# Optimization experiments

Hardware: AMD Instinct MI355X
Metric: run time of the kernel (lower is better)

The kernel has to match this reference:

```python
import jax, jax.numpy as jnp
import numpy as np

B, T, D, H = 4, 2048, 1024, 16
HD = D // H  # head_dim = 64

def setup_inputs() -> dict:
    key = jax.random.key(0)
    k1, k2, k3 = jax.random.split(key, 3)
    x = jax.random.normal(k1, (B, T, D), dtype=jnp.float32)
    Wqkv = jax.random.normal(k2, (D, 3 * D), dtype=jnp.float32) * (D ** -0.5)
    Wout = jax.random.normal(k3, (D, D), dtype=jnp.float32) * (D ** -0.5)
    return {"x": x, "Wqkv": Wqkv, "Wout": Wout}

def reference(x, Wqkv, Wout):
    Bb, Tt, C = x.shape
    qkv = x @ Wqkv  # [B,T,3D]
    qkv = qkv.reshape(Bb, Tt, 3, H, HD)
    q, k, v = qkv[:, :, 0], qkv[:, :, 1], qkv[:, :, 2]  # each [B,T,H,HD]
    scale = 1.0 / np.sqrt(HD)
    # scores [B,H,T,T]
    attn = jnp.einsum('bqhd,bkhd->bhqk', q, k) * scale
    causal = jnp.tril(jnp.ones((Tt, Tt), dtype=bool))
    attn = jnp.where(causal[None, None], attn, -jnp.inf)
    attn = jax.nn.softmax(attn, axis=-1)
    out = jnp.einsum('bhqk,bkhd->bqhd', attn, v).reshape(Bb, Tt, C)
    return out @ Wout
```

## Files before the change

### kernel.cpp

```cpp
#include <hip/hip_runtime.h>
#include <hip/hip_bf16.h>

#define T_SEQ 2048
#define NBATCH 4
#define NHEAD 16
#define HDIM 64
#define DMODEL 1024

typedef __bf16 bf16x8 __attribute__((ext_vector_type(8)));
typedef float f32x4 __attribute__((ext_vector_type(4)));
typedef float f32x16 __attribute__((ext_vector_type(16)));

__device__ __forceinline__ unsigned short f2bf(float f) {
  unsigned int u = __builtin_bit_cast(unsigned int, f);
  u += 0x7fffu + ((u >> 16) & 1u);
  return (unsigned short)(u >> 16);
}

__device__ __forceinline__ float fexp2(float x) {
  float r;
  asm("v_exp_f32 %0, %1" : "=v"(r) : "v"(x));
  return r;
}

__device__ __forceinline__ void async_cp16(void* lds, const void* g) {
  __builtin_amdgcn_global_load_lds((const __attribute__((address_space(1))) void*)g,
                                   (__attribute__((address_space(3))) void*)lds,
                                   16, 0, 0);
}

__global__ __launch_bounds__(256) void conv_bf16_k(const float* __restrict__ in,
                                                   unsigned short* __restrict__ out, int n) {
  int i = (blockIdx.x * 256 + threadIdx.x) * 4;
  if (i >= n) return;
  float4 v = *(const float4*)(in + i);
  ushort4 o;
  o.x = f2bf(v.x); o.y = f2bf(v.y); o.z = f2bf(v.z); o.w = f2bf(v.w);
  *(ushort4*)(out + i) = o;
}

__global__ __launch_bounds__(256) void transpose_bf16_k(const float* __restrict__ in,
                                                        unsigned short* __restrict__ out,
                                                        int R, int C) {
  __shared__ float tile[32][33];
  int c0 = blockIdx.x * 32, r0 = blockIdx.y * 32;
  int tx = threadIdx.x, ty = threadIdx.y;
#pragma unroll
  for (int j = 0; j < 32; j += 8)
    tile[ty + j][tx] = in[(size_t)(r0 + ty + j) * C + c0 + tx];
  __syncthreads();
#pragma unroll
  for (int j = 0; j < 32; j += 8)
    out[(size_t)(c0 + ty + j) * R + r0 + tx] = f2bf(tile[tx][ty + j]);
}

__global__ __launch_bounds__(512, 1) void gemm1_v3_k(const unsigned short* __restrict__ A,
                                                     const unsigned short* __restrict__ Bt,
                                                     unsigned short* __restrict__ Qb,
                                                     unsigned short* __restrict__ Kb,
                                                     unsigned short* __restrict__ Vt) {
  __shared__ uint4 ldsv[7168];
  char* lds = (char*)ldsv;
  const int t = threadIdx.x;
  const int w = t >> 6, lane = t & 63;
  const int lr = lane & 15, lg = lane >> 4;
  const int wr = w >> 1, wc = w & 1;
  const int bid = blockIdx.x;
  const int wid = (bid & 7) * 64 + (bid >> 3);
  const int m0 = (wid >> 4) * 256, n0 = (wid & 15) * 192;

  const int row0 = t >> 3;
  const int colc0 = (t & 7) ^ (row0 & 7);
  const int stU = w * 1024;

  const unsigned short* Abase = A + (size_t)(m0 + row0) * 1024 + colc0 * 8;
  const unsigned short* Bbase = Bt + (size_t)(n0 + row0) * 1024 + colc0 * 8;

#define STGA(pb, h, kt)                                                          \
  async_cp16(lds + (pb) + (h) * 8192 + stU,                                      \
             Abase + (size_t)(h) * 64 * 1024 + (kt) * 64)
#define STGB(pb, s, kt)                                                          \
  async_cp16(lds + (pb) + 32768 + (s) * 8192 + stU,                              \
             Bbase + (size_t)(s) * 64 * 1024 + (kt) * 64)
#define VM3() asm volatile("s_waitcnt vmcnt(3)" ::: "memory")
#define BAR()                                                                    \
  {                                                                              \
    __builtin_amdgcn_s_barrier();                                                \
    __builtin_amdgcn_sched_barrier(0);                                           \
  }

  f32x4 acc[4][6];
#pragma unroll
  for (int mi = 0; mi < 4; ++mi)
#pragma unroll
    for (int ni = 0; ni < 6; ++ni) acc[mi][ni] = (f32x4){0.f, 0.f, 0.f, 0.f};

  STGA(0, 0, 0); STGA(0, 1, 0); STGA(0, 2, 0); STGA(0, 3, 0);
  STGB(0, 0, 0); STGB(0, 1, 0); STGB(0, 2, 0);
  STGB(57344, 0, 1); STGB(57344, 1, 1); STGB(57344, 2, 1);
  VM3();
  BAR();

  bf16x8 bfr[6][2], af[2];

#define LDB(pb)                                                                      \
  {                                                                                  \
    _Pragma("unroll") for (int ni = 0; ni < 6; ++ni) _Pragma("unroll")               \
        for (int kk = 0; kk < 2; ++kk) {                                             \
      int rrow = wc * 96 + ni * 16 + lr;                                             \
      int cc = (kk * 4 + lg) ^ (lr & 7);                                             \
      bfr[ni][kk] = *(const bf16x8*)(lds + (pb) + 32768 + rrow * 128 + cc * 16);     \
    }                                                                                \
  }
#define LDA(Q, pb)                                                                   \
  {                                                                                  \
    _Pragma("unroll") for (int kk = 0; kk < 2; ++kk) {                               \
      int rrow = wr * 64 + (Q) * 16 + lr;                                            \
      int cc = (kk * 4 + lg) ^ (lr & 7);                                             \
      af[kk] = *(const bf16x8*)(lds + (pb) + rrow * 128 + cc * 16);                  \
    }                                                                                \
  }
#define MM(Q)                                                                        \
  {                                                                                  \
    __builtin_amdgcn_s_setprio(1);                                                   \
    _Pragma("unroll") for (int kk = 0; kk < 2; ++kk) _Pragma("unroll")               \
        for (int ni = 0; ni < 6; ++ni) acc[Q][ni] =                                  \
            __builtin_amdgcn_mfma_f32_16x16x32_bf16(af[kk], bfr[ni][kk],             \
                                                    acc[Q][ni], 0, 0, 0);            \
    __builtin_amdgcn_s_setprio(0);                                                   \
  }

  const int P0 = 0, P1 = 57344;
  for (int I = 0; I < 8; ++I) {
    const int t1 = 2 * I + 1;
    const int t2 = (2 * I + 2 < 16) ? 2 * I + 2 : 15;
    const int t3 = (2 * I + 3 < 16) ? 2 * I + 3 : 15;
    LDB(P0); LDA(0, P0); STGA(P1, 0, t1); STGA(P1, 1, t1); BAR(); MM(0); BAR();
    LDA(1, P0); STGA(P1, 2, t1); STGA(P1, 3, t1); BAR(); MM(1); BAR();
    LDA(2, P0); STGB(P0, 0, t2); STGB(P0, 1, t2); BAR(); MM(2); BAR();
    LDA(3, P0); STGB(P0, 2, t2); BAR(); MM(3);
    VM3();
    BAR();
    LDB(P1); LDA(0, P1); STGA(P0, 0, t2); STGA(P0, 1, t2); BAR(); MM(0); BAR();
    LDA(1, P1); STGA(P0, 2, t2); STGA(P0, 3, t2); BAR(); MM(1); BAR();
    LDA(2, P1); STGB(P1, 0, t3); STGB(P1, 1, t3); BAR(); MM(2); BAR();
    LDA(3, P1); STGB(P1, 2, t3); BAR(); MM(3);
    VM3();
    BAR();
  }

#pragma unroll
  for (int mi = 0; mi < 4; ++mi) {
#pragma unroll
    for (int ni = 0; ni < 6; ++ni) {
      int gm = m0 + wr * 64 + mi * 16 + lg * 4;
      int gn = n0 + wc * 96 + ni * 16 + lr;
      f32x4 v = acc[mi][ni];
      int b = gm >> 11, tt = gm & 2047;
      int sel = gn >> 10, rem = gn & 1023;
      int h = rem >> 6, hd = rem & 63;
      int bh = b * NHEAD + h;
      if (sel == 0) {
        unsigned short* p = Qb + ((size_t)bh * T_SEQ + tt) * HDIM + hd;
#pragma unroll
        for (int r = 0; r < 4; ++r)
          p[(size_t)r * HDIM] = f2bf(v[r] * (0.125f * 1.44269504f));
      } else if (sel == 1) {
        unsigned short* p = Kb + (size_t)bh * T_SEQ * HDIM + (tt >> 5) * 2048 +
                            (hd >> 4) * 512 + ((hd >> 3) & 1) * 256 + (tt & 31) * 8 +
                            (hd & 7);
#pragma unroll
        for (int r = 0; r < 4; ++r) p[r * 8] = f2bf(v[r]);
      } else {
        unsigned short* p = Vt + (size_t)bh * T_SEQ * HDIM + (tt >> 4) * 1024 +
                            ((tt >> 3) & 1) * 512 + (hd >> 5) * 256 + (hd & 31) * 8 +
                            (tt & 7);
        ushort4 o;
        o.x = f2bf(v[0]); o.y = f2bf(v[1]); o.z = f2bf(v[2]); o.w = f2bf(v[3]);
        *(ushort4*)p = o;
      }
    }
  }
#undef STGA
#undef STGB
#undef VM3
#undef BAR
#undef LDB
#undef LDA
#undef MM
}

template <int EPI, int NT>
__global__ __launch_bounds__(512, 1) void gemm_8ph2_k(const unsigned short* __restrict__ A,
                                                      const unsigned short* __restrict__ Bt,
                                                      unsigned short* __restrict__ Qb,
                                                      unsigned short* __restrict__ Kb,
                                                      unsigned short* __restrict__ Vt,
                                                      float* __restrict__ Cout) {
  __shared__ uint4 ldsv[6144];
  char* lds = (char*)ldsv;
  const int t = threadIdx.x;
  const int w = t >> 6, lane = t & 63;
  const int lr = lane & 15, lg = lane >> 4;
  const int wr = w >> 1, wc = w & 1;
  const int bid = blockIdx.x;
  const int perx = (NT * 32) / 8;
  const int wid = (bid & 7) * perx + (bid >> 3);
  const int m0 = (wid / NT) * 256, n0 = (wid % NT) * 128;

  const int row0 = t >> 3;
  const int colc0 = (t & 7) ^ (row0 & 7);
  const int stU = w * 1024;

  const unsigned short* Abase = A + (size_t)(m0 + row0) * 1024 + colc0 * 8;
  const unsigned short* Bbase = Bt + (size_t)(n0 + row0) * 1024 + colc0 * 8;

#define STGA(dst, h, kt)                                                        \
  {                                                                             \
    const unsigned short* _s = Abase + (size_t)(h) * 128 * 1024 + (kt) * 64;    \
    async_cp16(lds + (dst) + (h) * 16384 + stU, _s);                            \
    async_cp16(lds + (dst) + (h) * 16384 + stU + 8192, _s + 64 * 1024);         \
  }
#define STGB(dst, kt)                                                           \
  {                                                                             \
    const unsigned short* _s = Bbase + (kt) * 64;                               \
    async_cp16(lds + (dst) + 32768 + stU, _s);                                  \
    async_cp16(lds + (dst) + 32768 + stU + 8192, _s + 64 * 1024);               \
  }
#define VM2() asm volatile("s_waitcnt vmcnt(2)" ::: "memory")
#define BAR()                                                                   \
  {                                                                             \
    __builtin_amdgcn_s_barrier();                                               \
    __builtin_amdgcn_sched_barrier(0);                                          \
  }

  f32x4 acc[4][4];
#pragma unroll
  for (int mi = 0; mi < 4; ++mi)
#pragma unroll
    for (int ni = 0; ni < 4; ++ni) acc[mi][ni] = (f32x4){0.f, 0.f, 0.f, 0.f};

  STGA(0, 0, 0);
  STGA(0, 1, 0);
  STGB(0, 0);
  STGB(49152, 1);
  VM2();
  BAR();

  bf16x8 bfr[4][2], af[2][2];
  const int ldsAh = (wr >> 1) * 16384;
  const int arow0 = (wr & 1) * 64;
  const int brow0 = wc * 64;

#define LDB(pbase)                                                                   \
  {                                                                                  \
    _Pragma("unroll") for (int ni = 0; ni < 4; ++ni) _Pragma("unroll")               \
        for (int kk = 0; kk < 2; ++kk) {                                             \
      int rrow = brow0 + ni * 16 + lr;                                               \
      int cc = (kk * 4 + lg) ^ (lr & 7);                                             \
      bfr[ni][kk] = *(const bf16x8*)(lds + (pbase) + 32768 + rrow * 128 + cc * 16);  \
    }                                                                                \
  }
#define LDA(Q, pbase)                                                                \
  {                                                                                  \
    _Pragma("unroll") for (int m2 = 0; m2 < 2; ++m2) _Pragma("unroll")               \
        for (int kk = 0; kk < 2; ++kk) {                                             \
      int rrow = arow0 + (2 * (Q) + m2) * 16 + lr;                                   \
      int cc = (kk * 4 + lg) ^ (lr & 7);                                             \
      af[m2][kk] = *(const bf16x8*)(lds + (pbase) + ldsAh + rrow * 128 + cc * 16);   \
    }                                                                                \
  }
#define MM(Q)                                                                        \
  {                                                                                  \
    __builtin_amdgcn_s_setprio(1);                                                   \
    _Pragma("unroll") for (int m2 = 0; m2 < 2; ++m2) _Pragma("unroll")               \
        for (int kk = 0; kk < 2; ++kk) _Pragma("unroll") for (int ni = 0; ni < 4;    \
                                                              ++ni) acc[2 * (Q) +    \
                                                                        m2][ni] =    \
            __builtin_amdgcn_mfma_f32_16x16x32_bf16(af[m2][kk], bfr[ni][kk],         \
                                                    acc[2 * (Q) + m2][ni], 0, 0, 0); \
    __builtin_amdgcn_s_setprio(0);                                                   \
  }

  for (int I = 0; I < 8; ++I) {
    const int t1o = 2 * I + 1;
    const int t2e = (2 * I + 2 < 16) ? 2 * I + 2 : 15;
    const int t3o = (2 * I + 3 < 16) ? 2 * I + 3 : 15;
    LDB(0); LDA(0, 0); STGA(49152, 0, t1o); BAR(); MM(0); BAR();
    LDA(1, 0); STGA(49152, 1, t1o); STGB(0, t2e); BAR(); MM(1); VM2(); BAR();
    LDB(49152); LDA(0, 49152); STGA(0, 0, t2e); BAR(); MM(0); BAR();
    LDA(1, 49152); STGA(0, 1, t2e); STGB(49152, t3o); BAR(); MM(1); VM2(); BAR();
  }

#pragma unroll
  for (int mi = 0; mi < 4; ++mi) {
#pragma unroll
    for (int ni = 0; ni < 4; ++ni) {
      int gm = m0 + wr * 64 + mi * 16 + lg * 4;
      int gn = n0 + wc * 64 + ni * 16 + lr;
      f32x4 v = acc[mi][ni];
#pragma unroll
      for (int r = 0; r < 4; ++r) Cout[(size_t)(gm + r) * (NT * 128) + gn] = v[r];
    }
  }
#undef STGA
#undef STGB
#undef VM2
#undef BAR
#undef LDB
#undef LDA
#undef MM
}

#define PVJJ(Sv, B, JJ, Oa, Obb)                                                              \
  {                                                                                           \
    unsigned w0, w1, w2, w3;                                                                  \
    asm("v_cvt_pk_bf16_f32 %0, %1, %2" : "=v"(w0) : "v"(Sv[B + 0]), "v"(Sv[B + 1]));          \
    asm("v_cvt_pk_bf16_f32 %0, %1, %2" : "=v"(w1) : "v"(Sv[B + 2]), "v"(Sv[B + 3]));          \
    asm("v_cvt_pk_bf16_f32 %0, %1, %2" : "=v"(w2) : "v"(Sv[B + 4]), "v"(Sv[B + 5]));          \
    asm("v_cvt_pk_bf16_f32 %0, %1, %2" : "=v"(w3) : "v"(Sv[B + 6]), "v"(Sv[B + 7]));          \
    asm("v_permlane32_swap_b32 %0, %1" : "+v"(w0), "+v"(w2));                                 \
    asm("v_permlane32_swap_b32 %0, %1" : "+v"(w1), "+v"(w3));                                 \
    union { unsigned u[4]; bf16x8 v; } pf;                                                    \
    pf.u[0] = w0; pf.u[1] = w1; pf.u[2] = w2; pf.u[3] = w3;                                   \
    bf16x8 vfa = *(const bf16x8*)(bv + (JJ) * 2048 + hi * 1024 + lq * 16);                    \
    bf16x8 vfb = *(const bf16x8*)(bv + (JJ) * 2048 + hi * 1024 + lq * 16 + 512);              \
    __builtin_amdgcn_s_setprio(1);                                                            \
    Oa = __builtin_amdgcn_mfma_f32_32x32x16_bf16(vfa, pf.v, Oa, 0, 0, 0);                     \
    Obb = __builtin_amdgcn_mfma_f32_32x32x16_bf16(vfb, pf.v, Obb, 0, 0, 0);                   \
    __builtin_amdgcn_s_setprio(0);                                                            \
  }

__global__ __launch_bounds__(512, 2) void attn_fwd9_k(const unsigned short* __restrict__ Qb,
                                                      const unsigned short* __restrict__ Kb,
                                                      const unsigned short* __restrict__ Vt,
                                                      unsigned short* __restrict__ Ob) {
  __shared__ char lds[32768];
  const int tid = threadIdx.x;
  const int w = tid >> 6, lane = tid & 63;
  const int lq = lane & 31, hi = lane >> 5;
  const int bid = blockIdx.x;
  const int xcd = bid & 7, i = bid >> 3;
  const int bh = xcd * 8 + (i & 7);
  const int s = (i < 32) ? 7 - (i >> 3) : (i >> 3) - 4;
  const int qb = s * 8 + w;
  const int qw = qb * 32;
  const int P = 4 * (s + 1);

  const unsigned short* Qp = Qb + (size_t)bh * T_SEQ * HDIM;
  const char* Ksrc = (const char*)(Kb + (size_t)bh * T_SEQ * HDIM);
  const char* Vsrc = (const char*)(Vt + (size_t)bh * T_SEQ * HDIM);
  const int b = bh >> 4, h = bh & 15;

#define ASTG(bb, p)                                                                  \
  {                                                                                  \
    async_cp16(lds + (bb) * 16384 + w * 1024, Ksrc + (size_t)(p) * 8192 + tid * 16); \
    async_cp16(lds + (bb) * 16384 + 8192 + w * 1024,                                 \
               Vsrc + (size_t)(p) * 8192 + tid * 16);                                \
  }

  bf16x8 qf[4];
#pragma unroll
  for (int dj = 0; dj < 4; ++dj)
    qf[dj] = *(const bf16x8*)(Qp + (size_t)(qw + lq) * HDIM + dj * 16 + hi * 8);

  f32x16 O0, O1;
#pragma unroll
  for (int r = 0; r < 16; ++r) { O0[r] = 0.f; O1[r] = 0.f; }
  float m_run = -30000.0f, l_run = 0.f;

  auto smax_pair = [&](f32x16& S0, f32x16& S1) {
    float m8[8];
#pragma unroll
    for (int r = 0; r < 8; ++r)
      m8[r] = fmaxf(fmaxf(S0[r], S0[r + 8]), fmaxf(S1[r], S1[r + 8]));
#pragma unroll
    for (int r = 0; r < 4; ++r) m8[r] = fmaxf(m8[r], m8[r + 4]);
    float pmax = fmaxf(fmaxf(m8[0], m8[1]), fmaxf(m8[2], m8[3]));
    pmax = fmaxf(pmax, __shfl_xor(pmax, 32, 64));
    if (__any(pmax > m_run + 11.5f)) {
      float mn = fmaxf(m_run, pmax);
      float al = fexp2(m_run - mn);
      m_run = mn;
      l_run *= al;
#pragma unroll
      for (int r = 0; r < 16; ++r) { O0[r] *= al; O1[r] *= al; }
    }
#pragma unroll
    for (int r = 0; r < 16; ++r) {
      S0[r] = fexp2(S0[r] - m_run);
      S1[r] = fexp2(S1[r] - m_run);
    }
    float s8[8];
#pragma unroll
    for (int r = 0; r < 8; ++r) s8[r] = (S0[r] + S0[r + 8]) + (S1[r] + S1[r + 8]);
#pragma unroll
    for (int r = 0; r < 4; ++r) s8[r] += s8[r + 4];
    float ps = (s8[0] + s8[1]) + (s8[2] + s8[3]);
    ps += __shfl_xor(ps, 32, 64);
    l_run += ps;
  };

  auto smax_single = [&](f32x16& S0) {
    float m8[8];
#pragma unroll
    for (int r = 0; r < 8; ++r) m8[r] = fmaxf(S0[r], S0[r + 8]);
#pragma unroll
    for (int r = 0; r < 4; ++r) m8[r] = fmaxf(m8[r], m8[r + 4]);
    float pmax = fmaxf(fmaxf(m8[0], m8[1]), fmaxf(m8[2], m8[3]));
    pmax = fmaxf(pmax, __shfl_xor(pmax, 32, 64));
    if (__any(pmax > m_run + 11.5f)) {
      float mn = fmaxf(m_run, pmax);
      float al = fexp2(m_run - mn);
      m_run = mn;
      l_run *= al;
#pragma unroll
      for (int r = 0; r < 16; ++r) { O0[r] *= al; O1[r] *= al; }
    }
#pragma unroll
    for (int r = 0; r < 16; ++r) S0[r] = fexp2(S0[r] - m_run);
    float s8[8];
#pragma unroll
    for (int r = 0; r < 8; ++r) s8[r] = S0[r] + S0[r + 8];
#pragma unroll
    for (int r = 0; r < 4; ++r) s8[r] += s8[r + 4];
    float ps = (s8[0] + s8[1]) + (s8[2] + s8[3]);
    ps += __shfl_xor(ps, 32, 64);
    l_run += ps;
  };

  ASTG(0, 0);
  __syncthreads();

  for (int p = 0; p < P; ++p) {
    if (p + 1 < P) ASTG((p + 1) & 1, p + 1);
    const char* bk = lds + (p & 1) * 16384;
    const char* bv = bk + 8192;
    const int t0 = 2 * p, t1 = 2 * p + 1;
    if (t0 <= qb) {
      const bool v1 = (t1 <= qb);
      f32x16 S0, S1;
#pragma unroll
      for (int r = 0; r < 16; ++r) { S0[r] = 0.f; S1[r] = 0.f; }
      __builtin_amdgcn_s_setprio(1);
#pragma unroll
      for (int dj = 0; dj < 4; ++dj) {
        bf16x8 k0 = *(const bf16x8*)(bk + dj * 1024 + lane * 16);
        S0 = __builtin_amdgcn_mfma_f32_32x32x16_bf16(k0, qf[dj], S0, 0, 0, 0);
      }
      if (v1) {
#pragma unroll
        for (int dj = 0; dj < 4; ++dj) {
          bf16x8 k1 = *(const bf16x8*)(bk + 4096 + dj * 1024 + lane * 16);
          S1 = __builtin_amdgcn_mfma_f32_32x32x16_bf16(k1, qf[dj], S1, 0, 0, 0);
        }
      }
      __builtin_amdgcn_s_setprio(0);
      if (t0 == qb) {
#pragma unroll
        for (int r = 0; r < 16; ++r) {
          int kvl = (r & 3) + 8 * (r >> 2) + 4 * hi;
          S0[r] = (kvl > lq) ? -30000.0f : S0[r];
        }
      }
      if (v1 && t1 == qb) {
#pragma unroll
        for (int r = 0; r < 16; ++r) {
          int kvl = (r & 3) + 8 * (r >> 2) + 4 * hi;
          S1[r] = (kvl > lq) ? -30000.0f : S1[r];
        }
      }
      if (v1) {
        smax_pair(S0, S1);
        PVJJ(S0, 0, 0, O0, O1); PVJJ(S0, 8, 1, O0, O1);
        PVJJ(S1, 0, 2, O0, O1); PVJJ(S1, 8, 3, O0, O1);
      } else {
        smax_single(S0);
        PVJJ(S0, 0, 0, O0, O1); PVJJ(S0, 8, 1, O0, O1);
      }
    }
    __syncthreads();
  }

  const float linv = 1.0f / l_run;
  unsigned short* op = Ob + ((size_t)(b * T_SEQ + qw + lq)) * DMODEL + h * HDIM;
#pragma unroll
  for (int g = 0; g < 4; ++g) {
    ushort4 o;
    o.x = f2bf(O0[4 * g + 0] * linv);
    o.y = f2bf(O0[4 * g + 1] * linv);
    o.z = f2bf(O0[4 * g + 2] * linv);
    o.w = f2bf(O0[4 * g + 3] * linv);
    *(ushort4*)(op + 8 * g + 4 * hi) = o;
    ushort4 o2;
    o2.x = f2bf(O1[4 * g + 0] * linv);
    o2.y = f2bf(O1[4 * g + 1] * linv);
    o2.z = f2bf(O1[4 * g + 2] * linv);
    o2.w = f2bf(O1[4 * g + 3] * linv);
    *(ushort4*)(op + 32 + 8 * g + 4 * hi) = o2;
  }
#undef ASTG
}

extern "C" void kernel_launch(void* const* d_in, const int* in_sizes, int n_in,
                              void* d_out, int out_size, void* d_ws, size_t ws_size,
                              hipStream_t stream) {
  const float* x = (const float*)d_in[0];
  const float* Wqkv = (const float*)d_in[1];
  const float* Wout = (const float*)d_in[2];
  float* out = (float*)d_out;

  unsigned short* ws = (unsigned short*)d_ws;
  const size_t nx = (size_t)NBATCH * T_SEQ * DMODEL;
  unsigned short* xb    = ws;
  unsigned short* wqkvT = xb + nx;
  unsigned short* woutT = wqkvT + (size_t)3 * DMODEL * DMODEL;
  unsigned short* Qb    = woutT + (size_t)DMODEL * DMODEL;
  unsigned short* Kb    = Qb + nx;
  unsigned short* Vt    = Kb + nx;
  unsigned short* Ab    = Vt + nx;
  size_t need = 2ull * (5 * nx + 4ull * DMODEL * DMODEL);
  if (ws_size < need) return;

  conv_bf16_k<<<dim3((unsigned)(nx / 1024)), dim3(256), 0, stream>>>(x, xb, (int)nx);
  transpose_bf16_k<<<dim3(3 * DMODEL / 32, DMODEL / 32), dim3(32, 8), 0, stream>>>(
      Wqkv, wqkvT, DMODEL, 3 * DMODEL);
  transpose_bf16_k<<<dim3(DMODEL / 32, DMODEL / 32), dim3(32, 8), 0, stream>>>(
      Wout, woutT, DMODEL, DMODEL);
  gemm1_v3_k<<<dim3(512), dim3(512), 0, stream>>>(xb, wqkvT, Qb, Kb, Vt);
  attn_fwd9_k<<<dim3(512), dim3(512), 0, stream>>>(Qb, Kb, Vt, Ab);
  gemm_8ph2_k<1, 8><<<dim3(256), dim3(512), 0, stream>>>(Ab, woutT, nullptr, nullptr,
                                                         nullptr, out);
}
```

Measured before the change: 146.5 us.

## Merge prep kernels into one launch and halve barrier phases in QKV GEMM

The three preprocessing launches (x conversion to bf16 and the two weight transpose-conversions) are folded into a single kernel whose block index selects the job, removing two launch gaps. The QKV projection GEMM main loop is restructured from four barrier-separated MFMA phases per buffer to two, double-buffering A fragments so two M-subtiles are loaded and multiplied per phase. This cuts barrier count and groups the global-to-LDS stage issues, at the cost of extra registers for the second A fragment set and less fine-grained interleaving of loads with compute.

```diff
diff --git a/kernel.cpp b/kernel.cpp
--- a/kernel.cpp
+++ b/kernel.cpp
@@ -29,22 +29,36 @@
                                    16, 0, 0);
 }
 
-__global__ __launch_bounds__(256) void conv_bf16_k(const float* __restrict__ in,
-                                                   unsigned short* __restrict__ out, int n) {
-  int i = (blockIdx.x * 256 + threadIdx.x) * 4;
-  if (i >= n) return;
-  float4 v = *(const float4*)(in + i);
-  ushort4 o;
-  o.x = f2bf(v.x); o.y = f2bf(v.y); o.z = f2bf(v.z); o.w = f2bf(v.w);
-  *(ushort4*)(out + i) = o;
-}
-
-__global__ __launch_bounds__(256) void transpose_bf16_k(const float* __restrict__ in,
-                                                        unsigned short* __restrict__ out,
-                                                        int R, int C) {
+__global__ __launch_bounds__(256) void prep_k(const float* __restrict__ x,
+                                              const float* __restrict__ Wqkv,
+                                              const float* __restrict__ Wout,
+                                              unsigned short* __restrict__ xb,
+                                              unsigned short* __restrict__ wqkvT,
+                                              unsigned short* __restrict__ woutT) {
   __shared__ float tile[32][33];
-  int c0 = blockIdx.x * 32, r0 = blockIdx.y * 32;
-  int tx = threadIdx.x, ty = threadIdx.y;
+  const int bidx = blockIdx.x;
+  const int t = threadIdx.x;
+  if (bidx < 8192) {
+    int i = (bidx * 256 + t) * 4;
+    float4 v = *(const float4*)(x + i);
+    ushort4 o;
+    o.x = f2bf(v.x); o.y = f2bf(v.y); o.z = f2bf(v.z); o.w = f2bf(v.w);
+    *(ushort4*)(xb + i) = o;
+    return;
+  }
+  const float* in;
+  unsigned short* out;
+  int R, C, c0, r0;
+  if (bidx < 8192 + 3072) {
+    int tb = bidx - 8192;
+    in = Wqkv; out = wqkvT; R = 1024; C = 3072;
+    c0 = (tb % 96) * 32; r0 = (tb / 96) * 32;
+  } else {
+    int tb = bidx - 11264;
+    in = Wout; out = woutT; R = 1024; C = 1024;
+    c0 = (tb & 31) * 32; r0 = (tb >> 5) * 32;
+  }
+  const int tx = t & 31, ty = t >> 5;
 #pragma unroll
   for (int j = 0; j < 32; j += 8)
     tile[ty + j][tx] = in[(size_t)(r0 + ty + j) * C + c0 + tx];
@@ -54,7 +68,7 @@
     out[(size_t)(c0 + ty + j) * R + r0 + tx] = f2bf(tile[tx][ty + j]);
 }
 
-__global__ __launch_bounds__(512, 1) void gemm1_v3_k(const unsigned short* __restrict__ A,
+__global__ __launch_bounds__(512, 1) void gemm1_v4_k(const unsigned short* __restrict__ A,
                                                      const unsigned short* __restrict__ Bt,
                                                      unsigned short* __restrict__ Qb,
                                                      unsigned short* __restrict__ Kb,
@@ -101,7 +115,7 @@
   VM3();
   BAR();
 
-  bf16x8 bfr[6][2], af[2];
+  bf16x8 bfr[6][2], af[2][2];
 
 #define LDB(pb)                                                                      \
   {                                                                                  \
@@ -112,20 +126,20 @@
       bfr[ni][kk] = *(const bf16x8*)(lds + (pb) + 32768 + rrow * 128 + cc * 16);     \
     }                                                                                \
   }
-#define LDA(Q, pb)                                                                   \
+#define LDA(Q, pb, S)                                                                \
   {                                                                                  \
     _Pragma("unroll") for (int kk = 0; kk < 2; ++kk) {                               \
       int rrow = wr * 64 + (Q) * 16 + lr;                                            \
       int cc = (kk * 4 + lg) ^ (lr & 7);                                             \
-      af[kk] = *(const bf16x8*)(lds + (pb) + rrow * 128 + cc * 16);                  \
+      af[S][kk] = *(const bf16x8*)(lds + (pb) + rrow * 128 + cc * 16);               \
     }                                                                                \
   }
-#define MM(Q)                                                                        \
+#define MM(Q, S)                                                                     \
   {                                                                                  \
     __builtin_amdgcn_s_setprio(1);                                                   \
     _Pragma("unroll") for (int kk = 0; kk < 2; ++kk) _Pragma("unroll")               \
         for (int ni = 0; ni < 6; ++ni) acc[Q][ni] =                                  \
-            __builtin_amdgcn_mfma_f32_16x16x32_bf16(af[kk], bfr[ni][kk],             \
+            __builtin_amdgcn_mfma_f32_16x16x32_bf16(af[S][kk], bfr[ni][kk],          \
                                                     acc[Q][ni], 0, 0, 0);            \
     __builtin_amdgcn_s_setprio(0);                                                   \
   }
@@ -135,18 +149,20 @@
     const int t1 = 2 * I + 1;
     const int t2 = (2 * I + 2 < 16) ? 2 * I + 2 : 15;
     const int t3 = (2 * I + 3 < 16) ? 2 * I + 3 : 15;
-    LDB(P0); LDA(0, P0); STGA(P1, 0, t1); STGA(P1, 1, t1); BAR(); MM(0); BAR();
-    LDA(1, P0); STGA(P1, 2, t1); STGA(P1, 3, t1); BAR(); MM(1); BAR();
-    LDA(2, P0); STGB(P0, 0, t2); STGB(P0, 1, t2); BAR(); MM(2); BAR();
-    LDA(3, P0); STGB(P0, 2, t2); BAR(); MM(3);
-    VM3();
-    BAR();
-    LDB(P1); LDA(0, P1); STGA(P0, 0, t2); STGA(P0, 1, t2); BAR(); MM(0); BAR();
-    LDA(1, P1); STGA(P0, 2, t2); STGA(P0, 3, t2); BAR(); MM(1); BAR();
-    LDA(2, P1); STGB(P1, 0, t3); STGB(P1, 1, t3); BAR(); MM(2); BAR();
-    LDA(3, P1); STGB(P1, 2, t3); BAR(); MM(3);
-    VM3();
-    BAR();
+    LDB(P0); LDA(0, P0, 0); LDA(1, P0, 1);
+    STGA(P1, 0, t1); STGA(P1, 1, t1);
+    BAR(); MM(0, 0); MM(1, 1); BAR();
+    LDA(2, P0, 0); LDA(3, P0, 1);
+    STGA(P1, 2, t1); STGA(P1, 3, t1);
+    STGB(P0, 0, t2); STGB(P0, 1, t2); STGB(P0, 2, t2);
+    BAR(); MM(2, 0); MM(3, 1); VM3(); BAR();
+    LDB(P1); LDA(0, P1, 0); LDA(1, P1, 1);
+    STGA(P0, 0, t2); STGA(P0, 1, t2);
+    BAR(); MM(0, 0); MM(1, 1); BAR();
+    LDA(2, P1, 0); LDA(3, P1, 1);
+    STGA(P0, 2, t2); STGA(P0, 3, t2);
+    STGB(P1, 0, t3); STGB(P1, 1, t3); STGB(P1, 2, t3);
+    BAR(); MM(2, 0); MM(3, 1); VM3(); BAR();
   }
 
 #pragma unroll
@@ -522,12 +538,8 @@
   size_t need = 2ull * (5 * nx + 4ull * DMODEL * DMODEL);
   if (ws_size < need) return;
 
-  conv_bf16_k<<<dim3((unsigned)(nx / 1024)), dim3(256), 0, stream>>>(x, xb, (int)nx);
-  transpose_bf16_k<<<dim3(3 * DMODEL / 32, DMODEL / 32), dim3(32, 8), 0, stream>>>(
-      Wqkv, wqkvT, DMODEL, 3 * DMODEL);
-  transpose_bf16_k<<<dim3(DMODEL / 32, DMODEL / 32), dim3(32, 8), 0, stream>>>(
-      Wout, woutT, DMODEL, DMODEL);
-  gemm1_v3_k<<<dim3(512), dim3(512), 0, stream>>>(xb, wqkvT, Qb, Kb, Vt);
+  prep_k<<<dim3(12288), dim3(256), 0, stream>>>(x, Wqkv, Wout, xb, wqkvT, woutT);
+  gemm1_v4_k<<<dim3(512), dim3(512), 0, stream>>>(xb, wqkvT, Qb, Kb, Vt);
   attn_fwd9_k<<<dim3(512), dim3(512), 0, stream>>>(Qb, Kb, Vt, Ab);
   gemm_8ph2_k<1, 8><<<dim3(256), dim3(512), 0, stream>>>(Ab, woutT, nullptr, nullptr,
                                                          nullptr, out);
```

Result: no change. 145.0 us (-1.0%).
